# Kernel tuning notes

Hardware: AMD Instinct MI355X
Metric: run time of the kernel (lower is better)

Reference implementation:

```python
import jax, jax.numpy as jnp
import numpy as np

N = 100000   # nodes
E = 625000   # edges
D = 128      # feature / embedding dim
C = 40       # num classes
BN_EPS = 1e-5
L2_EPS = 1e-12


def setup_inputs() -> dict:
    key = jax.random.key(0)
    ks = jax.random.split(key, 8)
    s = 1.0 / np.sqrt(D)
    return {
        "x": jax.random.normal(ks[0], (N, D), dtype=jnp.float32),
        "edge_index": jax.random.randint(ks[1], (2, E), 0, N, dtype=jnp.int64),
        "W1": jax.random.normal(ks[2], (D, D), dtype=jnp.float32) * s,
        "b1": jnp.zeros((D,), jnp.float32),
        "W2": jax.random.normal(ks[3], (D, D), dtype=jnp.float32) * s,
        "b2": jnp.zeros((D,), jnp.float32),
        "W3": jax.random.normal(ks[4], (D, D), dtype=jnp.float32) * s,
        "b3": jnp.zeros((D,), jnp.float32),
        "g1": jnp.ones((D,), jnp.float32), "be1": jnp.zeros((D,), jnp.float32),
        "g2": jnp.ones((D,), jnp.float32), "be2": jnp.zeros((D,), jnp.float32),
        "g3": jnp.ones((D,), jnp.float32), "be3": jnp.zeros((D,), jnp.float32),
        "Wout": jax.random.normal(ks[5], (D, C), dtype=jnp.float32) * s,
        "bout": jnp.zeros((C,), jnp.float32),
    }


def _gcn_norm(edge_index, n):
    # PyG GCNConv default: add self loops, symmetric normalization
    loop = jnp.arange(n)
    src = jnp.concatenate([edge_index[0], loop])
    dst = jnp.concatenate([edge_index[1], loop])
    deg = jax.ops.segment_sum(jnp.ones_like(src, dtype=jnp.float32), dst, num_segments=n)
    dinv = jnp.where(deg > 0, jax.lax.rsqrt(deg), 0.0)
    norm = dinv[src] * dinv[dst]  # [E+N]
    return src, dst, norm


def _gcn_conv(x, W, b, src, dst, norm, n):
    h = x @ W                                # [N, D]
    msg = h[src] * norm[:, None]             # gather, [E+N, D]
    out = jax.ops.segment_sum(msg, dst, num_segments=n)  # scatter-add
    return out + b


def _bn(x, g, b):
    mu = jnp.mean(x, axis=0)
    var = jnp.var(x, axis=0)
    return (x - mu) * jax.lax.rsqrt(var + BN_EPS) * g + b


def _l2norm(x):
    n = jnp.sqrt(jnp.sum(x * x, axis=1, keepdims=True))
    return x / jnp.maximum(n, L2_EPS)


def reference(x, edge_index, W1, b1, W2, b2, W3, b3,
              g1, be1, g2, be2, g3, be3, Wout, bout):
    n = x.shape[0]
    src, dst, norm = _gcn_norm(edge_index, n)

    h = jax.nn.relu(_bn(_gcn_conv(x, W1, b1, src, dst, norm, n), g1, be1))
    h = _l2norm(h)
    r = h
    h = jax.nn.relu(_bn(_gcn_conv(h, W2, b2, src, dst, norm, n), g2, be2))
    h = _l2norm(h + r)
    r = h
    h = jax.nn.relu(_bn(_gcn_conv(h, W3, b3, src, dst, norm, n), g3, be3))
    h = _l2norm(h + r)

    return h @ Wout + bout  # node classification logits [N, C]
```

## Files before the change

### kernel.cpp

```cpp
#include <hip/hip_runtime.h>
#include <math.h>

#define DD 128
#define COUT 40
#define BN_EPS 1e-5f
#define L2_EPS 1e-12f

typedef __attribute__((ext_vector_type(8))) short bf16x8;
typedef __attribute__((ext_vector_type(4))) float f32x4;

static __device__ inline unsigned short f2bf(float f) {
    unsigned int x = __float_as_uint(f);
    unsigned int r = (x + 0x7FFFu + ((x >> 16) & 1u)) >> 16;
    return (unsigned short)r;
}
static __device__ inline float bf2f(unsigned short u) {
    return __uint_as_float(((unsigned int)u) << 16);
}


__global__ void k_prep(const float* __restrict__ W1, const float* __restrict__ W2,
                       const float* __restrict__ W3, const float* __restrict__ Wout,
                       unsigned short* __restrict__ wb,
                       unsigned short* __restrict__ wob,
                       float* __restrict__ stats,
                       int* __restrict__ zbase, int zn) {
    int b = blockIdx.x;
    if (b < 24) {
        int wi = b >> 3;
        const float* W = (wi == 0) ? W1 : (wi == 1) ? W2 : W3;
        unsigned short* out = wb + wi * 16384;
        int idx = (b & 7) * 256 + threadIdx.x;
        int kc = idx >> 9;
        int cc = (idx >> 6) & 7;
        int lane = idx & 63;
        int n = cc * 16 + (lane & 15);
        int kb = kc * 32 + (lane >> 4) * 8;
        unsigned short tmp[8];
#pragma unroll
        for (int j = 0; j < 8; j++) tmp[j] = f2bf(W[(size_t)(kb + j) * DD + n]);
        *(uint4*)&out[(size_t)idx * 8] = *(const uint4*)tmp;
    } else if (b < 27) {
        int idx = (b - 24) * 256 + threadIdx.x;
        int kc = idx / 192;
        int rem = idx % 192;
        int cc = rem >> 6;
        int lane = rem & 63;
        int n = cc * 16 + (lane & 15);
        int kb = kc * 32 + (lane >> 4) * 8;
        unsigned short tmp[8];
#pragma unroll
        for (int j = 0; j < 8; j++)
            tmp[j] = (n < COUT) ? f2bf(Wout[(size_t)(kb + j) * COUT + n]) : 0;
        *(uint4*)&wob[(size_t)idx * 8] = *(const uint4*)tmp;
    } else if (b == 27) {
        stats[threadIdx.x] = 0.f;
        stats[256 + threadIdx.x] = 0.f;
        stats[512 + threadIdx.x] = 0.f;
    } else {
        int idx = (b - 28) * 2048 + threadIdx.x * 8;
        if (idx + 8 <= zn) {
            *(int4*)&zbase[idx] = make_int4(0, 0, 0, 0);
            *(int4*)&zbase[idx + 4] = make_int4(0, 0, 0, 0);
        }
    }
}

__global__ void k_hist(const int* ei, int E, int* deg) {
    int i = blockIdx.x * blockDim.x + threadIdx.x;
    if (i < E) atomicAdd(&deg[ei[E + i]], 1);
}

__global__ void k_scan_a(const int* deg, int* row_ptr, int* bsum, float* dinv, int n) {
    __shared__ int s[256];
    int t = threadIdx.x;
    int idx = blockIdx.x * 256 + t;
    int v = (idx < n) ? deg[idx] + 1 : 0;
    if (idx < n) dinv[idx] = rsqrtf((float)v);
    s[t] = v; __syncthreads();
    for (int off = 1; off < 256; off <<= 1) {
        int x = (t >= off) ? s[t - off] : 0;
        __syncthreads(); s[t] += x; __syncthreads();
    }
    if (idx <= n) row_ptr[idx] = s[t] - v;
    if (t == 255) bsum[blockIdx.x] = s[255];
}

__global__ void k_scan_b(const int* bsum, int* boff, int nb) {
    __shared__ int s[512];
    int t = threadIdx.x;
    int v = (t < nb) ? bsum[t] : 0;
    s[t] = v; __syncthreads();
    for (int off = 1; off < 512; off <<= 1) {
        int x = (t >= off) ? s[t - off] : 0;
        __syncthreads(); s[t] += x; __syncthreads();
    }
    if (t < nb) boff[t] = s[t] - v;
}

__global__ void k_fill(const int* ei, int E, int n, const int* row_ptr, const int* boff,
                       int* fill, int* colidx) {
    int i = blockIdx.x * blockDim.x + threadIdx.x;
    int total = E + n;
    if (i >= total) return;
    int u, v;
    if (i < E) { u = ei[i]; v = ei[E + i]; }
    else { u = i - E; v = u; }
    int p = atomicAdd(&fill[v], 1);
    int pos = row_ptr[v] + boff[v >> 8] + p;
    colidx[pos] = u;
}


__global__ __launch_bounds__(256) void k_gemm0(const float* __restrict__ A,
                                               const unsigned short* __restrict__ Wb,
                                               const float* __restrict__ dinv,
                                               unsigned short* __restrict__ C, int nrows) {
    __shared__ __align__(16) unsigned short Ws[16384];
    const int tid = threadIdx.x;
    for (int i = tid; i < 2048; i += 256)
        ((uint4*)Ws)[i] = ((const uint4*)Wb)[i];
    __syncthreads();

    const int wv = tid >> 6;
    const int lane = tid & 63;
    const int R0 = blockIdx.x * 64 + wv * 16;
    if (R0 >= nrows) return;
    const int m = lane & 15, q = lane >> 4;
    int rr = R0 + m; if (rr >= nrows) rr = nrows - 1;
    const float* Ar = A + (size_t)rr * DD + q * 8;

    bf16x8 af[4];
#pragma unroll
    for (int kc = 0; kc < 4; kc++) {
        float4 lo = *(const float4*)(Ar + kc * 32);
        float4 hi = *(const float4*)(Ar + kc * 32 + 4);
        unsigned short t[8];
        t[0] = f2bf(lo.x); t[1] = f2bf(lo.y); t[2] = f2bf(lo.z); t[3] = f2bf(lo.w);
        t[4] = f2bf(hi.x); t[5] = f2bf(hi.y); t[6] = f2bf(hi.z); t[7] = f2bf(hi.w);
        af[kc] = *(const bf16x8*)t;
    }

    f32x4 acc[8];
#pragma unroll
    for (int cc = 0; cc < 8; cc++) acc[cc] = (f32x4){0.f, 0.f, 0.f, 0.f};
#pragma unroll
    for (int kc = 0; kc < 4; kc++)
#pragma unroll
        for (int cc = 0; cc < 8; cc++) {
            bf16x8 b = *(const bf16x8*)&Ws[(size_t)((kc * 8 + cc) * 64 + lane) * 8];
            acc[cc] = __builtin_amdgcn_mfma_f32_16x16x32_bf16(af[kc], b, acc[cc], 0, 0, 0);
        }

    float dr[4];
#pragma unroll
    for (int i = 0; i < 4; i++) {
        int r = R0 + q * 4 + i;
        dr[i] = (r < nrows) ? dinv[r] : 0.f;
    }
#pragma unroll
    for (int cc = 0; cc < 8; cc++)
#pragma unroll
        for (int i = 0; i < 4; i++) {
            int r = R0 + q * 4 + i;
            if (r < nrows) C[(size_t)r * DD + cc * 16 + m] = f2bf(acc[cc][i] * dr[i]);
        }
}

__global__ void k_agg(const unsigned short* __restrict__ lin, const int* __restrict__ row_ptr,
                      const int* __restrict__ boff, const int* __restrict__ colidx,
                      const float* __restrict__ dinv, const float* __restrict__ bias,
                      unsigned short* __restrict__ outb, int n) {
    int lane = threadIdx.x;
    int half = lane >> 5;
    int li = lane & 31;
    int v = blockIdx.x * 8 + threadIdx.y * 2 + half;
    if (v >= n) return;
    int c = li * 4;
    int s = row_ptr[v] + boff[v >> 8];
    int e = row_ptr[v + 1] + boff[(v + 1) >> 8];
    float dv = dinv[v];
    float4 a0 = make_float4(0.f, 0.f, 0.f, 0.f);
    float4 a1 = make_float4(0.f, 0.f, 0.f, 0.f);
    float4 a2 = make_float4(0.f, 0.f, 0.f, 0.f);
    float4 a3 = make_float4(0.f, 0.f, 0.f, 0.f);
    int j = s;
    for (; j + 3 < e; j += 4) {
        int u0 = colidx[j], u1 = colidx[j + 1], u2 = colidx[j + 2], u3 = colidx[j + 3];
        ushort4 t0 = *(const ushort4*)&lin[(size_t)u0 * DD + c];
        ushort4 t1 = *(const ushort4*)&lin[(size_t)u1 * DD + c];
        ushort4 t2 = *(const ushort4*)&lin[(size_t)u2 * DD + c];
        ushort4 t3 = *(const ushort4*)&lin[(size_t)u3 * DD + c];
        a0.x += bf2f(t0.x); a0.y += bf2f(t0.y); a0.z += bf2f(t0.z); a0.w += bf2f(t0.w);
        a1.x += bf2f(t1.x); a1.y += bf2f(t1.y); a1.z += bf2f(t1.z); a1.w += bf2f(t1.w);
        a2.x += bf2f(t2.x); a2.y += bf2f(t2.y); a2.z += bf2f(t2.z); a2.w += bf2f(t2.w);
        a3.x += bf2f(t3.x); a3.y += bf2f(t3.y); a3.z += bf2f(t3.z); a3.w += bf2f(t3.w);
    }
    for (; j < e; ++j) {
        int u = colidx[j];
        ushort4 t = *(const ushort4*)&lin[(size_t)u * DD + c];
        a0.x += bf2f(t.x); a0.y += bf2f(t.y); a0.z += bf2f(t.z); a0.w += bf2f(t.w);
    }
    float4 bi = *(const float4*)&bias[c];
    float ox = bi.x + dv * (a0.x + a1.x + a2.x + a3.x);
    float oy = bi.y + dv * (a0.y + a1.y + a2.y + a3.y);
    float oz = bi.z + dv * (a0.z + a1.z + a2.z + a3.z);
    float ow = bi.w + dv * (a0.w + a1.w + a2.w + a3.w);
    ushort4 o;
    o.x = f2bf(ox); o.y = f2bf(oy); o.z = f2bf(oz); o.w = f2bf(ow);
    *(ushort4*)&outb[(size_t)v * DD + c] = o;
}

__global__ __launch_bounds__(256) void k_bnstats(const unsigned short* __restrict__ X, int n,
                                                 float* __restrict__ stats) {
    int cg = (threadIdx.x & 31) * 4;
    int rg = threadIdx.x >> 5;
    float s0 = 0, s1 = 0, s2 = 0, s3 = 0;
    float q0 = 0, q1 = 0, q2 = 0, q3 = 0;
    for (int r = blockIdx.x * 8 + rg; r < n; r += gridDim.x * 8) {
        ushort4 xv = *(const ushort4*)&X[(size_t)r * DD + cg];
        float x0 = bf2f(xv.x), x1 = bf2f(xv.y), x2 = bf2f(xv.z), x3 = bf2f(xv.w);
        s0 += x0; s1 += x1; s2 += x2; s3 += x3;
        q0 += x0 * x0; q1 += x1 * x1; q2 += x2 * x2; q3 += x3 * x3;
    }
    __shared__ float sh[8][128];
    __shared__ float qh[8][128];
    sh[rg][cg] = s0; sh[rg][cg + 1] = s1; sh[rg][cg + 2] = s2; sh[rg][cg + 3] = s3;
    qh[rg][cg] = q0; qh[rg][cg + 1] = q1; qh[rg][cg + 2] = q2; qh[rg][cg + 3] = q3;
    __syncthreads();
    if (threadIdx.x < 128) {
        float a = 0, b = 0;
        for (int g = 0; g < 8; g++) { a += sh[g][threadIdx.x]; b += qh[g][threadIdx.x]; }
        atomicAdd(&stats[threadIdx.x], a);
        atomicAdd(&stats[128 + threadIdx.x], b);
    }
}

template <bool HAS_RES>
__global__ __launch_bounds__(256) void k_fused(const unsigned short* __restrict__ aggX,
                                               const float* __restrict__ stats,
                                               const float* __restrict__ g,
                                               const float* __restrict__ be, float inv_n,
                                               const unsigned short* __restrict__ resb,
                                               const unsigned short* __restrict__ Wb,
                                               const float* __restrict__ dinv,
                                               unsigned short* __restrict__ hbf_out,
                                               unsigned short* __restrict__ linb_out,
                                               int nrows) {
    __shared__ __align__(16) unsigned short Ws[16384];
    __shared__ float ssl[256];
    const int tid = threadIdx.x;
    for (int i = tid; i < 2048; i += 256)
        ((uint4*)Ws)[i] = ((const uint4*)Wb)[i];
    if (tid < 128) {
        float mu = stats[tid] * inv_n;
        float var = stats[128 + tid] * inv_n - mu * mu;
        float sc = g[tid] * rsqrtf(var + BN_EPS);
        ssl[tid] = sc;
        ssl[128 + tid] = be[tid] - mu * sc;
    }
    __syncthreads();

    const int wv = tid >> 6;
    const int lane = tid & 63;
    const int R0 = blockIdx.x * 64 + wv * 16;
    if (R0 >= nrows) return;
    const int m = lane & 15, q = lane >> 4;
    int rr = R0 + m; if (rr >= nrows) rr = nrows - 1;
    const unsigned short* Ar = aggX + (size_t)rr * DD + q * 8;
    const unsigned short* Rr = HAS_RES ? resb + (size_t)rr * DD + q * 8 : nullptr;

    float y[4][8];
    float sq = 0.f;
#pragma unroll
    for (int kc = 0; kc < 4; kc++) {
        ushort4 lo = *(const ushort4*)(Ar + kc * 32);
        ushort4 hi = *(const ushort4*)(Ar + kc * 32 + 4);
        unsigned short av[8] = {lo.x, lo.y, lo.z, lo.w, hi.x, hi.y, hi.z, hi.w};
        int c0 = kc * 32 + q * 8;
        float4 sc0 = *(const float4*)&ssl[c0];
        float4 sc1 = *(const float4*)&ssl[c0 + 4];
        float4 sh0 = *(const float4*)&ssl[128 + c0];
        float4 sh1 = *(const float4*)&ssl[128 + c0 + 4];
        float scv[8] = {sc0.x, sc0.y, sc0.z, sc0.w, sc1.x, sc1.y, sc1.z, sc1.w};
        float shv[8] = {sh0.x, sh0.y, sh0.z, sh0.w, sh1.x, sh1.y, sh1.z, sh1.w};
        if (HAS_RES) {
            ushort4 rl = *(const ushort4*)(Rr + kc * 32);
            ushort4 rh = *(const ushort4*)(Rr + kc * 32 + 4);
            unsigned short rv[8] = {rl.x, rl.y, rl.z, rl.w, rh.x, rh.y, rh.z, rh.w};
#pragma unroll
            for (int j = 0; j < 8; j++) {
                float yy = fmaxf(bf2f(av[j]) * scv[j] + shv[j], 0.f) + bf2f(rv[j]);
                y[kc][j] = yy; sq += yy * yy;
            }
        } else {
#pragma unroll
            for (int j = 0; j < 8; j++) {
                float yy = fmaxf(bf2f(av[j]) * scv[j] + shv[j], 0.f);
                y[kc][j] = yy; sq += yy * yy;
            }
        }
    }
    sq += __shfl_xor(sq, 16, 64);
    sq += __shfl_xor(sq, 32, 64);
    float inv = 1.f / fmaxf(sqrtf(sq), L2_EPS);

    bf16x8 af[4];
#pragma unroll
    for (int kc = 0; kc < 4; kc++) {
        unsigned short t[8];
#pragma unroll
        for (int j = 0; j < 8; j++) t[j] = f2bf(y[kc][j] * inv);
        af[kc] = *(const bf16x8*)t;
        *(bf16x8*)&hbf_out[(size_t)rr * DD + q * 8 + kc * 32] = af[kc];
    }

    f32x4 acc[8];
#pragma unroll
    for (int cc = 0; cc < 8; cc++) acc[cc] = (f32x4){0.f, 0.f, 0.f, 0.f};
#pragma unroll
    for (int kc = 0; kc < 4; kc++)
#pragma unroll
        for (int cc = 0; cc < 8; cc++) {
            bf16x8 b = *(const bf16x8*)&Ws[(size_t)((kc * 8 + cc) * 64 + lane) * 8];
            acc[cc] = __builtin_amdgcn_mfma_f32_16x16x32_bf16(af[kc], b, acc[cc], 0, 0, 0);
        }

    float dr[4];
#pragma unroll
    for (int i = 0; i < 4; i++) {
        int r = R0 + q * 4 + i;
        dr[i] = (r < nrows) ? dinv[r] : 0.f;
    }
#pragma unroll
    for (int cc = 0; cc < 8; cc++)
#pragma unroll
        for (int i = 0; i < 4; i++) {
            int r = R0 + q * 4 + i;
            if (r < nrows) linb_out[(size_t)r * DD + cc * 16 + m] = f2bf(acc[cc][i] * dr[i]);
        }
}

__global__ __launch_bounds__(256) void k_outfused(const unsigned short* __restrict__ aggX,
                                                  const float* __restrict__ stats,
                                                  const float* __restrict__ g,
                                                  const float* __restrict__ be, float inv_n,
                                                  const unsigned short* __restrict__ resb,
                                                  const unsigned short* __restrict__ wob,
                                                  const float* __restrict__ bout,
                                                  float* __restrict__ C, int nrows) {
    __shared__ __align__(16) unsigned short Ws[6144];
    __shared__ float ssl[256];
    const int tid = threadIdx.x;
    for (int i = tid; i < 768; i += 256)
        ((uint4*)Ws)[i] = ((const uint4*)wob)[i];
    if (tid < 128) {
        float mu = stats[tid] * inv_n;
        float var = stats[128 + tid] * inv_n - mu * mu;
        float sc = g[tid] * rsqrtf(var + BN_EPS);
        ssl[tid] = sc;
        ssl[128 + tid] = be[tid] - mu * sc;
    }
    __syncthreads();

    const int wv = tid >> 6;
    const int lane = tid & 63;
    const int R0 = blockIdx.x * 64 + wv * 16;
    if (R0 >= nrows) return;
    const int m = lane & 15, q = lane >> 4;
    int rr = R0 + m; if (rr >= nrows) rr = nrows - 1;
    const unsigned short* Ar = aggX + (size_t)rr * DD + q * 8;
    const unsigned short* Rr = resb + (size_t)rr * DD + q * 8;

    float y[4][8];
    float sq = 0.f;
#pragma unroll
    for (int kc = 0; kc < 4; kc++) {
        ushort4 lo = *(const ushort4*)(Ar + kc * 32);
        ushort4 hi = *(const ushort4*)(Ar + kc * 32 + 4);
        ushort4 rl = *(const ushort4*)(Rr + kc * 32);
        ushort4 rh = *(const ushort4*)(Rr + kc * 32 + 4);
        unsigned short av[8] = {lo.x, lo.y, lo.z, lo.w, hi.x, hi.y, hi.z, hi.w};
        unsigned short rv[8] = {rl.x, rl.y, rl.z, rl.w, rh.x, rh.y, rh.z, rh.w};
        int c0 = kc * 32 + q * 8;
        float4 sc0 = *(const float4*)&ssl[c0];
        float4 sc1 = *(const float4*)&ssl[c0 + 4];
        float4 sh0 = *(const float4*)&ssl[128 + c0];
        float4 sh1 = *(const float4*)&ssl[128 + c0 + 4];
        float scv[8] = {sc0.x, sc0.y, sc0.z, sc0.w, sc1.x, sc1.y, sc1.z, sc1.w};
        float shv[8] = {sh0.x, sh0.y, sh0.z, sh0.w, sh1.x, sh1.y, sh1.z, sh1.w};
#pragma unroll
        for (int j = 0; j < 8; j++) {
            float yy = fmaxf(bf2f(av[j]) * scv[j] + shv[j], 0.f) + bf2f(rv[j]);
            y[kc][j] = yy; sq += yy * yy;
        }
    }
    sq += __shfl_xor(sq, 16, 64);
    sq += __shfl_xor(sq, 32, 64);
    float inv = 1.f / fmaxf(sqrtf(sq), L2_EPS);

    bf16x8 af[4];
#pragma unroll
    for (int kc = 0; kc < 4; kc++) {
        unsigned short t[8];
#pragma unroll
        for (int j = 0; j < 8; j++) t[j] = f2bf(y[kc][j] * inv);
        af[kc] = *(const bf16x8*)t;
    }

    f32x4 acc[3];
#pragma unroll
    for (int cc = 0; cc < 3; cc++) acc[cc] = (f32x4){0.f, 0.f, 0.f, 0.f};
#pragma unroll
    for (int kc = 0; kc < 4; kc++)
#pragma unroll
        for (int cc = 0; cc < 3; cc++) {
            bf16x8 b = *(const bf16x8*)&Ws[(size_t)((kc * 3 + cc) * 64 + lane) * 8];
            acc[cc] = __builtin_amdgcn_mfma_f32_16x16x32_bf16(af[kc], b, acc[cc], 0, 0, 0);
        }

#pragma unroll
    for (int cc = 0; cc < 3; cc++) {
        int col = cc * 16 + m;
        if (col < COUT) {
            float bb = bout[col];
#pragma unroll
            for (int i = 0; i < 4; i++) {
                int r = R0 + q * 4 + i;
                if (r < nrows) C[(size_t)r * COUT + col] = acc[cc][i] + bb;
            }
        }
    }
}


extern "C" void kernel_launch(void* const* d_in, const int* in_sizes, int n_in,
                              void* d_out, int out_size, void* d_ws, size_t ws_size,
                              hipStream_t stream) {
    const float* x    = (const float*)d_in[0];
    const int*   ei   = (const int*)d_in[1];
    const float* W1   = (const float*)d_in[2];
    const float* b1   = (const float*)d_in[3];
    const float* W2   = (const float*)d_in[4];
    const float* b2   = (const float*)d_in[5];
    const float* W3   = (const float*)d_in[6];
    const float* b3   = (const float*)d_in[7];
    const float* g1   = (const float*)d_in[8];
    const float* be1  = (const float*)d_in[9];
    const float* g2   = (const float*)d_in[10];
    const float* be2  = (const float*)d_in[11];
    const float* g3   = (const float*)d_in[12];
    const float* be3  = (const float*)d_in[13];
    const float* Wout = (const float*)d_in[14];
    const float* bout = (const float*)d_in[15];
    float* out = (float*)d_out;

    const int N = in_sizes[0] / DD;
    const int E = in_sizes[1] / 2;
    const int NNZ = E + N;

    char* w = (char*)d_ws;
    unsigned short* linb = (unsigned short*)w; w += (size_t)N * DD * sizeof(unsigned short);
    unsigned short* aggA = (unsigned short*)w; w += (size_t)N * DD * sizeof(unsigned short);
    unsigned short* aggB = (unsigned short*)w; w += (size_t)N * DD * sizeof(unsigned short);
    unsigned short* hbf1 = (unsigned short*)w; w += (size_t)N * DD * sizeof(unsigned short);
    unsigned short* hbf2 = (unsigned short*)w; w += (size_t)N * DD * sizeof(unsigned short);
    unsigned short* wb   = (unsigned short*)w; w += 3 * 16384 * sizeof(unsigned short);
    unsigned short* wob  = (unsigned short*)w; w += 6144 * sizeof(unsigned short);
    int* colidx  = (int*)w;                    w += (size_t)NNZ * sizeof(int);
    int* deg     = (int*)w;                    w += (size_t)N * sizeof(int);
    int* fill    = (int*)w;                    w += (size_t)N * sizeof(int);
    int* row_ptr = (int*)w;                    w += (size_t)(N + 1) * sizeof(int);
    float* dinv  = (float*)w;                  w += (size_t)N * sizeof(float);
    int* bsum    = (int*)w;                    w += 512 * sizeof(int);
    int* boff    = (int*)w;                    w += 512 * sizeof(int);
    float* stats = (float*)w;                  w += 768 * sizeof(float);

    const int NB = (N + 1 + 255) / 256;
    const int STATS_GRID = 128;
    const int ZN = 2 * N;
    const int ZBLK = (ZN + 2047) / 2048;

    k_prep<<<28 + ZBLK, 256, 0, stream>>>(W1, W2, W3, Wout, wb, wob, stats, deg, ZN);
    k_hist<<<(E + 255) / 256, 256, 0, stream>>>(ei, E, deg);
    k_scan_a<<<NB, 256, 0, stream>>>(deg, row_ptr, bsum, dinv, N);
    k_scan_b<<<1, 512, 0, stream>>>(bsum, boff, NB);
    k_fill<<<(NNZ + 255) / 256, 256, 0, stream>>>(ei, E, N, row_ptr, boff, fill, colidx);

    int gemmGrid = (N + 63) / 64;
    dim3 aggGrid((N + 7) / 8);
    dim3 aggBlk(64, 4);
    float inv_n = 1.0f / (float)N;

    k_gemm0<<<gemmGrid, 256, 0, stream>>>(x, wb, dinv, linb, N);
    k_agg<<<aggGrid, aggBlk, 0, stream>>>(linb, row_ptr, boff, colidx, dinv, b1, aggA, N);
    k_bnstats<<<STATS_GRID, 256, 0, stream>>>(aggA, N, stats);
    k_fused<false><<<gemmGrid, 256, 0, stream>>>(aggA, stats, g1, be1, inv_n,
                                                 nullptr, wb + 16384, dinv, hbf1, linb, N);
    k_agg<<<aggGrid, aggBlk, 0, stream>>>(linb, row_ptr, boff, colidx, dinv, b2, aggB, N);
    k_bnstats<<<STATS_GRID, 256, 0, stream>>>(aggB, N, stats + 256);
    k_fused<true><<<gemmGrid, 256, 0, stream>>>(aggB, stats + 256, g2, be2, inv_n,
                                                hbf1, wb + 32768, dinv, hbf2, linb, N);
    k_agg<<<aggGrid, aggBlk, 0, stream>>>(linb, row_ptr, boff, colidx, dinv, b3, aggA, N);
    k_bnstats<<<STATS_GRID, 256, 0, stream>>>(aggA, N, stats + 512);
    k_outfused<<<gemmGrid, 256, 0, stream>>>(aggA, stats + 512, g3, be3, inv_n,
                                             hbf2, wob, bout, out, N);
}
```

Before: 483.0 us.

## Merge all GCN stages into one cooperative persistent kernel with grid syncs

Replaces the sequence of roughly fifteen separate launches (prep, histogram, scans, fill, GEMM, aggregation, BN stats, fused layers) with a single cooperative kernel. It runs grid-stride stages separated by grid-wide barriers. BN statistics are now accumulated inside the aggregation stage through shared-memory atomics, which removes the separate stats passes over the aggregated features. This cuts launch overhead and one full read of the features per layer. In exchange it adds grid-sync costs, limits the grid to occupancy times the CU count, and makes host-side device property queries on every call.

```diff
diff --git a/kernel.cpp b/kernel.cpp
--- a/kernel.cpp
+++ b/kernel.cpp
@@ -1,5 +1,8 @@
 #include <hip/hip_runtime.h>
+#include <hip/hip_cooperative_groups.h>
 #include <math.h>
+
+namespace cg = cooperative_groups;
 
 #define DD 128
 #define COUT 40
@@ -18,240 +21,96 @@
     return __uint_as_float(((unsigned int)u) << 16);
 }
 
-
-__global__ void k_prep(const float* __restrict__ W1, const float* __restrict__ W2,
-                       const float* __restrict__ W3, const float* __restrict__ Wout,
-                       unsigned short* __restrict__ wb,
-                       unsigned short* __restrict__ wob,
-                       float* __restrict__ stats,
-                       int* __restrict__ zbase, int zn) {
-    int b = blockIdx.x;
-    if (b < 24) {
-        int wi = b >> 3;
-        const float* W = (wi == 0) ? W1 : (wi == 1) ? W2 : W3;
-        unsigned short* out = wb + wi * 16384;
-        int idx = (b & 7) * 256 + threadIdx.x;
-        int kc = idx >> 9;
-        int cc = (idx >> 6) & 7;
-        int lane = idx & 63;
-        int n = cc * 16 + (lane & 15);
-        int kb = kc * 32 + (lane >> 4) * 8;
-        unsigned short tmp[8];
-#pragma unroll
-        for (int j = 0; j < 8; j++) tmp[j] = f2bf(W[(size_t)(kb + j) * DD + n]);
-        *(uint4*)&out[(size_t)idx * 8] = *(const uint4*)tmp;
-    } else if (b < 27) {
-        int idx = (b - 24) * 256 + threadIdx.x;
-        int kc = idx / 192;
-        int rem = idx % 192;
-        int cc = rem >> 6;
-        int lane = rem & 63;
-        int n = cc * 16 + (lane & 15);
-        int kb = kc * 32 + (lane >> 4) * 8;
-        unsigned short tmp[8];
-#pragma unroll
-        for (int j = 0; j < 8; j++)
-            tmp[j] = (n < COUT) ? f2bf(Wout[(size_t)(kb + j) * COUT + n]) : 0;
-        *(uint4*)&wob[(size_t)idx * 8] = *(const uint4*)tmp;
-    } else if (b == 27) {
-        stats[threadIdx.x] = 0.f;
-        stats[256 + threadIdx.x] = 0.f;
-        stats[512 + threadIdx.x] = 0.f;
-    } else {
-        int idx = (b - 28) * 2048 + threadIdx.x * 8;
-        if (idx + 8 <= zn) {
-            *(int4*)&zbase[idx] = make_int4(0, 0, 0, 0);
-            *(int4*)&zbase[idx + 4] = make_int4(0, 0, 0, 0);
-        }
-    }
-}
-
-__global__ void k_hist(const int* ei, int E, int* deg) {
-    int i = blockIdx.x * blockDim.x + threadIdx.x;
-    if (i < E) atomicAdd(&deg[ei[E + i]], 1);
-}
-
-__global__ void k_scan_a(const int* deg, int* row_ptr, int* bsum, float* dinv, int n) {
-    __shared__ int s[256];
-    int t = threadIdx.x;
-    int idx = blockIdx.x * 256 + t;
-    int v = (idx < n) ? deg[idx] + 1 : 0;
-    if (idx < n) dinv[idx] = rsqrtf((float)v);
-    s[t] = v; __syncthreads();
-    for (int off = 1; off < 256; off <<= 1) {
-        int x = (t >= off) ? s[t - off] : 0;
-        __syncthreads(); s[t] += x; __syncthreads();
-    }
-    if (idx <= n) row_ptr[idx] = s[t] - v;
-    if (t == 255) bsum[blockIdx.x] = s[255];
-}
-
-__global__ void k_scan_b(const int* bsum, int* boff, int nb) {
-    __shared__ int s[512];
-    int t = threadIdx.x;
-    int v = (t < nb) ? bsum[t] : 0;
-    s[t] = v; __syncthreads();
-    for (int off = 1; off < 512; off <<= 1) {
-        int x = (t >= off) ? s[t - off] : 0;
-        __syncthreads(); s[t] += x; __syncthreads();
-    }
-    if (t < nb) boff[t] = s[t] - v;
-}
-
-__global__ void k_fill(const int* ei, int E, int n, const int* row_ptr, const int* boff,
-                       int* fill, int* colidx) {
-    int i = blockIdx.x * blockDim.x + threadIdx.x;
-    int total = E + n;
-    if (i >= total) return;
-    int u, v;
-    if (i < E) { u = ei[i]; v = ei[E + i]; }
-    else { u = i - E; v = u; }
-    int p = atomicAdd(&fill[v], 1);
-    int pos = row_ptr[v] + boff[v >> 8] + p;
-    colidx[pos] = u;
-}
-
-
-__global__ __launch_bounds__(256) void k_gemm0(const float* __restrict__ A,
-                                               const unsigned short* __restrict__ Wb,
-                                               const float* __restrict__ dinv,
-                                               unsigned short* __restrict__ C, int nrows) {
-    __shared__ __align__(16) unsigned short Ws[16384];
+struct MegaParams {
+    const float* x; const int* ei;
+    const float *W1, *b1, *W2, *b2, *W3, *b3;
+    const float *g1, *be1, *g2, *be2, *g3, *be3;
+    const float *Wout, *bout;
+    float* out;
+    unsigned short *linb, *aggA, *aggB, *hbf1, *hbf2, *wb, *wob;
+    int *colidx, *deg, *fill, *row_ptr;
+    float* dinv;
+    int *bsum, *boff;
+    float* stats;
+    int N, E, NB;
+};
+
+
+static __device__ __forceinline__ void st_agg(const unsigned short* __restrict__ lin,
+                                              const int* __restrict__ row_ptr,
+                                              const int* __restrict__ boff,
+                                              const int* __restrict__ colidx,
+                                              const float* __restrict__ dinv,
+                                              const float* __restrict__ bias,
+                                              unsigned short* __restrict__ outb,
+                                              float* __restrict__ gstats,
+                                              float* lstats, int N) {
     const int tid = threadIdx.x;
-    for (int i = tid; i < 2048; i += 256)
-        ((uint4*)Ws)[i] = ((const uint4*)Wb)[i];
+    lstats[tid] = 0.f;
     __syncthreads();
-
-    const int wv = tid >> 6;
-    const int lane = tid & 63;
-    const int R0 = blockIdx.x * 64 + wv * 16;
-    if (R0 >= nrows) return;
-    const int m = lane & 15, q = lane >> 4;
-    int rr = R0 + m; if (rr >= nrows) rr = nrows - 1;
-    const float* Ar = A + (size_t)rr * DD + q * 8;
-
-    bf16x8 af[4];
-#pragma unroll
-    for (int kc = 0; kc < 4; kc++) {
-        float4 lo = *(const float4*)(Ar + kc * 32);
-        float4 hi = *(const float4*)(Ar + kc * 32 + 4);
-        unsigned short t[8];
-        t[0] = f2bf(lo.x); t[1] = f2bf(lo.y); t[2] = f2bf(lo.z); t[3] = f2bf(lo.w);
-        t[4] = f2bf(hi.x); t[5] = f2bf(hi.y); t[6] = f2bf(hi.z); t[7] = f2bf(hi.w);
-        af[kc] = *(const bf16x8*)t;
-    }
-
-    f32x4 acc[8];
-#pragma unroll
-    for (int cc = 0; cc < 8; cc++) acc[cc] = (f32x4){0.f, 0.f, 0.f, 0.f};
-#pragma unroll
-    for (int kc = 0; kc < 4; kc++)
-#pragma unroll
-        for (int cc = 0; cc < 8; cc++) {
-            bf16x8 b = *(const bf16x8*)&Ws[(size_t)((kc * 8 + cc) * 64 + lane) * 8];
-            acc[cc] = __builtin_amdgcn_mfma_f32_16x16x32_bf16(af[kc], b, acc[cc], 0, 0, 0);
-        }
-
-    float dr[4];
-#pragma unroll
-    for (int i = 0; i < 4; i++) {
-        int r = R0 + q * 4 + i;
-        dr[i] = (r < nrows) ? dinv[r] : 0.f;
-    }
-#pragma unroll
-    for (int cc = 0; cc < 8; cc++)
-#pragma unroll
-        for (int i = 0; i < 4; i++) {
-            int r = R0 + q * 4 + i;
-            if (r < nrows) C[(size_t)r * DD + cc * 16 + m] = f2bf(acc[cc][i] * dr[i]);
-        }
-}
-
-__global__ void k_agg(const unsigned short* __restrict__ lin, const int* __restrict__ row_ptr,
-                      const int* __restrict__ boff, const int* __restrict__ colidx,
-                      const float* __restrict__ dinv, const float* __restrict__ bias,
-                      unsigned short* __restrict__ outb, int n) {
-    int lane = threadIdx.x;
-    int half = lane >> 5;
-    int li = lane & 31;
-    int v = blockIdx.x * 8 + threadIdx.y * 2 + half;
-    if (v >= n) return;
-    int c = li * 4;
-    int s = row_ptr[v] + boff[v >> 8];
-    int e = row_ptr[v + 1] + boff[(v + 1) >> 8];
-    float dv = dinv[v];
-    float4 a0 = make_float4(0.f, 0.f, 0.f, 0.f);
-    float4 a1 = make_float4(0.f, 0.f, 0.f, 0.f);
-    float4 a2 = make_float4(0.f, 0.f, 0.f, 0.f);
-    float4 a3 = make_float4(0.f, 0.f, 0.f, 0.f);
-    int j = s;
-    for (; j + 3 < e; j += 4) {
-        int u0 = colidx[j], u1 = colidx[j + 1], u2 = colidx[j + 2], u3 = colidx[j + 3];
-        ushort4 t0 = *(const ushort4*)&lin[(size_t)u0 * DD + c];
-        ushort4 t1 = *(const ushort4*)&lin[(size_t)u1 * DD + c];
-        ushort4 t2 = *(const ushort4*)&lin[(size_t)u2 * DD + c];
-        ushort4 t3 = *(const ushort4*)&lin[(size_t)u3 * DD + c];
-        a0.x += bf2f(t0.x); a0.y += bf2f(t0.y); a0.z += bf2f(t0.z); a0.w += bf2f(t0.w);
-        a1.x += bf2f(t1.x); a1.y += bf2f(t1.y); a1.z += bf2f(t1.z); a1.w += bf2f(t1.w);
-        a2.x += bf2f(t2.x); a2.y += bf2f(t2.y); a2.z += bf2f(t2.z); a2.w += bf2f(t2.w);
-        a3.x += bf2f(t3.x); a3.y += bf2f(t3.y); a3.z += bf2f(t3.z); a3.w += bf2f(t3.w);
-    }
-    for (; j < e; ++j) {
-        int u = colidx[j];
-        ushort4 t = *(const ushort4*)&lin[(size_t)u * DD + c];
-        a0.x += bf2f(t.x); a0.y += bf2f(t.y); a0.z += bf2f(t.z); a0.w += bf2f(t.w);
-    }
-    float4 bi = *(const float4*)&bias[c];
-    float ox = bi.x + dv * (a0.x + a1.x + a2.x + a3.x);
-    float oy = bi.y + dv * (a0.y + a1.y + a2.y + a3.y);
-    float oz = bi.z + dv * (a0.z + a1.z + a2.z + a3.z);
-    float ow = bi.w + dv * (a0.w + a1.w + a2.w + a3.w);
-    ushort4 o;
-    o.x = f2bf(ox); o.y = f2bf(oy); o.z = f2bf(oz); o.w = f2bf(ow);
-    *(ushort4*)&outb[(size_t)v * DD + c] = o;
-}
-
-__global__ __launch_bounds__(256) void k_bnstats(const unsigned short* __restrict__ X, int n,
-                                                 float* __restrict__ stats) {
-    int cg = (threadIdx.x & 31) * 4;
-    int rg = threadIdx.x >> 5;
-    float s0 = 0, s1 = 0, s2 = 0, s3 = 0;
-    float q0 = 0, q1 = 0, q2 = 0, q3 = 0;
-    for (int r = blockIdx.x * 8 + rg; r < n; r += gridDim.x * 8) {
-        ushort4 xv = *(const ushort4*)&X[(size_t)r * DD + cg];
-        float x0 = bf2f(xv.x), x1 = bf2f(xv.y), x2 = bf2f(xv.z), x3 = bf2f(xv.w);
-        s0 += x0; s1 += x1; s2 += x2; s3 += x3;
-        q0 += x0 * x0; q1 += x1 * x1; q2 += x2 * x2; q3 += x3 * x3;
-    }
-    __shared__ float sh[8][128];
-    __shared__ float qh[8][128];
-    sh[rg][cg] = s0; sh[rg][cg + 1] = s1; sh[rg][cg + 2] = s2; sh[rg][cg + 3] = s3;
-    qh[rg][cg] = q0; qh[rg][cg + 1] = q1; qh[rg][cg + 2] = q2; qh[rg][cg + 3] = q3;
+    const int slot = (tid >> 6) * 2 + ((tid & 63) >> 5);
+    const int c = (tid & 31) * 4;
+    float s0 = 0, s1 = 0, s2 = 0, s3 = 0, q0 = 0, q1 = 0, q2 = 0, q3 = 0;
+    const int VB = (N + 7) / 8;
+    for (int vb = blockIdx.x; vb < VB; vb += gridDim.x) {
+        int v = vb * 8 + slot;
+        if (v >= N) continue;
+        int s = row_ptr[v] + boff[v >> 8];
+        int e = row_ptr[v + 1] + boff[(v + 1) >> 8];
+        float dv = dinv[v];
+        float4 a0 = make_float4(0.f, 0.f, 0.f, 0.f);
+        float4 a1 = make_float4(0.f, 0.f, 0.f, 0.f);
+        float4 a2 = make_float4(0.f, 0.f, 0.f, 0.f);
+        float4 a3 = make_float4(0.f, 0.f, 0.f, 0.f);
+        int j = s;
+        for (; j + 3 < e; j += 4) {
+            int u0 = colidx[j], u1 = colidx[j + 1], u2 = colidx[j + 2], u3 = colidx[j + 3];
+            ushort4 t0 = *(const ushort4*)&lin[(size_t)u0 * DD + c];
+            ushort4 t1 = *(const ushort4*)&lin[(size_t)u1 * DD + c];
+            ushort4 t2 = *(const ushort4*)&lin[(size_t)u2 * DD + c];
+            ushort4 t3 = *(const ushort4*)&lin[(size_t)u3 * DD + c];
+            a0.x += bf2f(t0.x); a0.y += bf2f(t0.y); a0.z += bf2f(t0.z); a0.w += bf2f(t0.w);
+            a1.x += bf2f(t1.x); a1.y += bf2f(t1.y); a1.z += bf2f(t1.z); a1.w += bf2f(t1.w);
+            a2.x += bf2f(t2.x); a2.y += bf2f(t2.y); a2.z += bf2f(t2.z); a2.w += bf2f(t2.w);
+            a3.x += bf2f(t3.x); a3.y += bf2f(t3.y); a3.z += bf2f(t3.z); a3.w += bf2f(t3.w);
+        }
+        for (; j < e; ++j) {
+            int u = colidx[j];
+            ushort4 t = *(const ushort4*)&lin[(size_t)u * DD + c];
+            a0.x += bf2f(t.x); a0.y += bf2f(t.y); a0.z += bf2f(t.z); a0.w += bf2f(t.w);
+        }
+        float4 bi = *(const float4*)&bias[c];
+        float ox = bi.x + dv * (a0.x + a1.x + a2.x + a3.x);
+        float oy = bi.y + dv * (a0.y + a1.y + a2.y + a3.y);
+        float oz = bi.z + dv * (a0.z + a1.z + a2.z + a3.z);
+        float ow = bi.w + dv * (a0.w + a1.w + a2.w + a3.w);
+        s0 += ox; s1 += oy; s2 += oz; s3 += ow;
+        q0 += ox * ox; q1 += oy * oy; q2 += oz * oz; q3 += ow * ow;
+        ushort4 o;
+        o.x = f2bf(ox); o.y = f2bf(oy); o.z = f2bf(oz); o.w = f2bf(ow);
+        *(ushort4*)&outb[(size_t)v * DD + c] = o;
+    }
+    atomicAdd(&lstats[c], s0); atomicAdd(&lstats[c + 1], s1);
+    atomicAdd(&lstats[c + 2], s2); atomicAdd(&lstats[c + 3], s3);
+    atomicAdd(&lstats[128 + c], q0); atomicAdd(&lstats[128 + c + 1], q1);
+    atomicAdd(&lstats[128 + c + 2], q2); atomicAdd(&lstats[128 + c + 3], q3);
     __syncthreads();
-    if (threadIdx.x < 128) {
-        float a = 0, b = 0;
-        for (int g = 0; g < 8; g++) { a += sh[g][threadIdx.x]; b += qh[g][threadIdx.x]; }
-        atomicAdd(&stats[threadIdx.x], a);
-        atomicAdd(&stats[128 + threadIdx.x], b);
-    }
+    atomicAdd(&gstats[tid], lstats[tid]);
 }
 
 template <bool HAS_RES>
-__global__ __launch_bounds__(256) void k_fused(const unsigned short* __restrict__ aggX,
-                                               const float* __restrict__ stats,
-                                               const float* __restrict__ g,
-                                               const float* __restrict__ be, float inv_n,
-                                               const unsigned short* __restrict__ resb,
-                                               const unsigned short* __restrict__ Wb,
-                                               const float* __restrict__ dinv,
-                                               unsigned short* __restrict__ hbf_out,
-                                               unsigned short* __restrict__ linb_out,
-                                               int nrows) {
-    __shared__ __align__(16) unsigned short Ws[16384];
-    __shared__ float ssl[256];
+static __device__ __forceinline__ void st_fused(const unsigned short* __restrict__ aggX,
+                                                const float* __restrict__ stats,
+                                                const float* __restrict__ g,
+                                                const float* __restrict__ be, float inv_n,
+                                                const unsigned short* __restrict__ resb,
+                                                const unsigned short* __restrict__ Wb,
+                                                const float* __restrict__ dinv,
+                                                unsigned short* __restrict__ hbf_out,
+                                                unsigned short* __restrict__ linb_out,
+                                                unsigned short* Ws, float* ssl, int N) {
     const int tid = threadIdx.x;
-    for (int i = tid; i < 2048; i += 256)
-        ((uint4*)Ws)[i] = ((const uint4*)Wb)[i];
+    for (int i = tid; i < 2048; i += 256) ((uint4*)Ws)[i] = ((const uint4*)Wb)[i];
     if (tid < 128) {
         float mu = stats[tid] * inv_n;
         float var = stats[128 + tid] * inv_n - mu * mu;
@@ -260,174 +119,304 @@
         ssl[128 + tid] = be[tid] - mu * sc;
     }
     __syncthreads();
-
-    const int wv = tid >> 6;
-    const int lane = tid & 63;
-    const int R0 = blockIdx.x * 64 + wv * 16;
-    if (R0 >= nrows) return;
-    const int m = lane & 15, q = lane >> 4;
-    int rr = R0 + m; if (rr >= nrows) rr = nrows - 1;
-    const unsigned short* Ar = aggX + (size_t)rr * DD + q * 8;
-    const unsigned short* Rr = HAS_RES ? resb + (size_t)rr * DD + q * 8 : nullptr;
-
-    float y[4][8];
-    float sq = 0.f;
-#pragma unroll
-    for (int kc = 0; kc < 4; kc++) {
-        ushort4 lo = *(const ushort4*)(Ar + kc * 32);
-        ushort4 hi = *(const ushort4*)(Ar + kc * 32 + 4);
-        unsigned short av[8] = {lo.x, lo.y, lo.z, lo.w, hi.x, hi.y, hi.z, hi.w};
-        int c0 = kc * 32 + q * 8;
-        float4 sc0 = *(const float4*)&ssl[c0];
-        float4 sc1 = *(const float4*)&ssl[c0 + 4];
-        float4 sh0 = *(const float4*)&ssl[128 + c0];
-        float4 sh1 = *(const float4*)&ssl[128 + c0 + 4];
-        float scv[8] = {sc0.x, sc0.y, sc0.z, sc0.w, sc1.x, sc1.y, sc1.z, sc1.w};
-        float shv[8] = {sh0.x, sh0.y, sh0.z, sh0.w, sh1.x, sh1.y, sh1.z, sh1.w};
-        if (HAS_RES) {
-            ushort4 rl = *(const ushort4*)(Rr + kc * 32);
-            ushort4 rh = *(const ushort4*)(Rr + kc * 32 + 4);
-            unsigned short rv[8] = {rl.x, rl.y, rl.z, rl.w, rh.x, rh.y, rh.z, rh.w};
-#pragma unroll
-            for (int j = 0; j < 8; j++) {
-                float yy = fmaxf(bf2f(av[j]) * scv[j] + shv[j], 0.f) + bf2f(rv[j]);
-                y[kc][j] = yy; sq += yy * yy;
-            }
-        } else {
-#pragma unroll
-            for (int j = 0; j < 8; j++) {
-                float yy = fmaxf(bf2f(av[j]) * scv[j] + shv[j], 0.f);
-                y[kc][j] = yy; sq += yy * yy;
-            }
-        }
-    }
-    sq += __shfl_xor(sq, 16, 64);
-    sq += __shfl_xor(sq, 32, 64);
-    float inv = 1.f / fmaxf(sqrtf(sq), L2_EPS);
-
-    bf16x8 af[4];
-#pragma unroll
-    for (int kc = 0; kc < 4; kc++) {
-        unsigned short t[8];
-#pragma unroll
-        for (int j = 0; j < 8; j++) t[j] = f2bf(y[kc][j] * inv);
-        af[kc] = *(const bf16x8*)t;
-        *(bf16x8*)&hbf_out[(size_t)rr * DD + q * 8 + kc * 32] = af[kc];
-    }
-
-    f32x4 acc[8];
-#pragma unroll
-    for (int cc = 0; cc < 8; cc++) acc[cc] = (f32x4){0.f, 0.f, 0.f, 0.f};
-#pragma unroll
-    for (int kc = 0; kc < 4; kc++)
-#pragma unroll
-        for (int cc = 0; cc < 8; cc++) {
-            bf16x8 b = *(const bf16x8*)&Ws[(size_t)((kc * 8 + cc) * 64 + lane) * 8];
-            acc[cc] = __builtin_amdgcn_mfma_f32_16x16x32_bf16(af[kc], b, acc[cc], 0, 0, 0);
-        }
-
-    float dr[4];
-#pragma unroll
-    for (int i = 0; i < 4; i++) {
-        int r = R0 + q * 4 + i;
-        dr[i] = (r < nrows) ? dinv[r] : 0.f;
-    }
-#pragma unroll
-    for (int cc = 0; cc < 8; cc++)
+    const int wv = tid >> 6, lane = tid & 63, m = lane & 15, q = lane >> 4;
+    const int NC = (N + 63) / 64;
+    for (int cb = blockIdx.x; cb < NC; cb += gridDim.x) {
+        int R0 = cb * 64 + wv * 16;
+        if (R0 >= N) continue;
+        int rr = R0 + m; if (rr >= N) rr = N - 1;
+        const unsigned short* Ar = aggX + (size_t)rr * DD + q * 8;
+        const unsigned short* Rr = HAS_RES ? resb + (size_t)rr * DD + q * 8 : nullptr;
+        float y[4][8];
+        float sq = 0.f;
+#pragma unroll
+        for (int kc = 0; kc < 4; kc++) {
+            ushort4 lo = *(const ushort4*)(Ar + kc * 32);
+            ushort4 hi = *(const ushort4*)(Ar + kc * 32 + 4);
+            unsigned short av[8] = {lo.x, lo.y, lo.z, lo.w, hi.x, hi.y, hi.z, hi.w};
+            int c0 = kc * 32 + q * 8;
+            float4 sc0 = *(const float4*)&ssl[c0];
+            float4 sc1 = *(const float4*)&ssl[c0 + 4];
+            float4 sh0 = *(const float4*)&ssl[128 + c0];
+            float4 sh1 = *(const float4*)&ssl[128 + c0 + 4];
+            float scv[8] = {sc0.x, sc0.y, sc0.z, sc0.w, sc1.x, sc1.y, sc1.z, sc1.w};
+            float shv[8] = {sh0.x, sh0.y, sh0.z, sh0.w, sh1.x, sh1.y, sh1.z, sh1.w};
+            if (HAS_RES) {
+                ushort4 rl = *(const ushort4*)(Rr + kc * 32);
+                ushort4 rh = *(const ushort4*)(Rr + kc * 32 + 4);
+                unsigned short rv[8] = {rl.x, rl.y, rl.z, rl.w, rh.x, rh.y, rh.z, rh.w};
+#pragma unroll
+                for (int j = 0; j < 8; j++) {
+                    float yy = fmaxf(bf2f(av[j]) * scv[j] + shv[j], 0.f) + bf2f(rv[j]);
+                    y[kc][j] = yy; sq += yy * yy;
+                }
+            } else {
+#pragma unroll
+                for (int j = 0; j < 8; j++) {
+                    float yy = fmaxf(bf2f(av[j]) * scv[j] + shv[j], 0.f);
+                    y[kc][j] = yy; sq += yy * yy;
+                }
+            }
+        }
+        sq += __shfl_xor(sq, 16, 64);
+        sq += __shfl_xor(sq, 32, 64);
+        float inv = 1.f / fmaxf(sqrtf(sq), L2_EPS);
+        bf16x8 af[4];
+#pragma unroll
+        for (int kc = 0; kc < 4; kc++) {
+            unsigned short t[8];
+#pragma unroll
+            for (int j = 0; j < 8; j++) t[j] = f2bf(y[kc][j] * inv);
+            af[kc] = *(const bf16x8*)t;
+            *(bf16x8*)&hbf_out[(size_t)rr * DD + q * 8 + kc * 32] = af[kc];
+        }
+        f32x4 acc[8];
+#pragma unroll
+        for (int cc = 0; cc < 8; cc++) acc[cc] = (f32x4){0.f, 0.f, 0.f, 0.f};
+#pragma unroll
+        for (int kc = 0; kc < 4; kc++)
+#pragma unroll
+            for (int cc = 0; cc < 8; cc++) {
+                bf16x8 b = *(const bf16x8*)&Ws[(size_t)((kc * 8 + cc) * 64 + lane) * 8];
+                acc[cc] = __builtin_amdgcn_mfma_f32_16x16x32_bf16(af[kc], b, acc[cc], 0, 0, 0);
+            }
+        float dr[4];
 #pragma unroll
         for (int i = 0; i < 4; i++) {
             int r = R0 + q * 4 + i;
-            if (r < nrows) linb_out[(size_t)r * DD + cc * 16 + m] = f2bf(acc[cc][i] * dr[i]);
-        }
-}
-
-__global__ __launch_bounds__(256) void k_outfused(const unsigned short* __restrict__ aggX,
-                                                  const float* __restrict__ stats,
-                                                  const float* __restrict__ g,
-                                                  const float* __restrict__ be, float inv_n,
-                                                  const unsigned short* __restrict__ resb,
-                                                  const unsigned short* __restrict__ wob,
-                                                  const float* __restrict__ bout,
-                                                  float* __restrict__ C, int nrows) {
-    __shared__ __align__(16) unsigned short Ws[6144];
-    __shared__ float ssl[256];
-    const int tid = threadIdx.x;
-    for (int i = tid; i < 768; i += 256)
-        ((uint4*)Ws)[i] = ((const uint4*)wob)[i];
-    if (tid < 128) {
-        float mu = stats[tid] * inv_n;
-        float var = stats[128 + tid] * inv_n - mu * mu;
-        float sc = g[tid] * rsqrtf(var + BN_EPS);
-        ssl[tid] = sc;
-        ssl[128 + tid] = be[tid] - mu * sc;
-    }
-    __syncthreads();
-
-    const int wv = tid >> 6;
-    const int lane = tid & 63;
-    const int R0 = blockIdx.x * 64 + wv * 16;
-    if (R0 >= nrows) return;
-    const int m = lane & 15, q = lane >> 4;
-    int rr = R0 + m; if (rr >= nrows) rr = nrows - 1;
-    const unsigned short* Ar = aggX + (size_t)rr * DD + q * 8;
-    const unsigned short* Rr = resb + (size_t)rr * DD + q * 8;
-
-    float y[4][8];
-    float sq = 0.f;
-#pragma unroll
-    for (int kc = 0; kc < 4; kc++) {
-        ushort4 lo = *(const ushort4*)(Ar + kc * 32);
-        ushort4 hi = *(const ushort4*)(Ar + kc * 32 + 4);
-        ushort4 rl = *(const ushort4*)(Rr + kc * 32);
-        ushort4 rh = *(const ushort4*)(Rr + kc * 32 + 4);
-        unsigned short av[8] = {lo.x, lo.y, lo.z, lo.w, hi.x, hi.y, hi.z, hi.w};
-        unsigned short rv[8] = {rl.x, rl.y, rl.z, rl.w, rh.x, rh.y, rh.z, rh.w};
-        int c0 = kc * 32 + q * 8;
-        float4 sc0 = *(const float4*)&ssl[c0];
-        float4 sc1 = *(const float4*)&ssl[c0 + 4];
-        float4 sh0 = *(const float4*)&ssl[128 + c0];
-        float4 sh1 = *(const float4*)&ssl[128 + c0 + 4];
-        float scv[8] = {sc0.x, sc0.y, sc0.z, sc0.w, sc1.x, sc1.y, sc1.z, sc1.w};
-        float shv[8] = {sh0.x, sh0.y, sh0.z, sh0.w, sh1.x, sh1.y, sh1.z, sh1.w};
-#pragma unroll
-        for (int j = 0; j < 8; j++) {
-            float yy = fmaxf(bf2f(av[j]) * scv[j] + shv[j], 0.f) + bf2f(rv[j]);
-            y[kc][j] = yy; sq += yy * yy;
-        }
-    }
-    sq += __shfl_xor(sq, 16, 64);
-    sq += __shfl_xor(sq, 32, 64);
-    float inv = 1.f / fmaxf(sqrtf(sq), L2_EPS);
-
-    bf16x8 af[4];
-#pragma unroll
-    for (int kc = 0; kc < 4; kc++) {
-        unsigned short t[8];
-#pragma unroll
-        for (int j = 0; j < 8; j++) t[j] = f2bf(y[kc][j] * inv);
-        af[kc] = *(const bf16x8*)t;
-    }
-
-    f32x4 acc[3];
-#pragma unroll
-    for (int cc = 0; cc < 3; cc++) acc[cc] = (f32x4){0.f, 0.f, 0.f, 0.f};
-#pragma unroll
-    for (int kc = 0; kc < 4; kc++)
-#pragma unroll
-        for (int cc = 0; cc < 3; cc++) {
-            bf16x8 b = *(const bf16x8*)&Ws[(size_t)((kc * 3 + cc) * 64 + lane) * 8];
-            acc[cc] = __builtin_amdgcn_mfma_f32_16x16x32_bf16(af[kc], b, acc[cc], 0, 0, 0);
-        }
-
-#pragma unroll
-    for (int cc = 0; cc < 3; cc++) {
-        int col = cc * 16 + m;
-        if (col < COUT) {
-            float bb = bout[col];
+            dr[i] = (r < N) ? dinv[r] : 0.f;
+        }
+#pragma unroll
+        for (int cc = 0; cc < 8; cc++)
 #pragma unroll
             for (int i = 0; i < 4; i++) {
                 int r = R0 + q * 4 + i;
-                if (r < nrows) C[(size_t)r * COUT + col] = acc[cc][i] + bb;
+                if (r < N) linb_out[(size_t)r * DD + cc * 16 + m] = f2bf(acc[cc][i] * dr[i]);
+            }
+    }
+}
+
+
+__global__ __launch_bounds__(256) void k_mega(MegaParams p) {
+    cg::grid_group grid = cg::this_grid();
+    const int tid = threadIdx.x;
+    const int gid = blockIdx.x * 256 + tid;
+    const int gsz = gridDim.x * 256;
+
+    __shared__ __align__(16) unsigned short Ws[16384];
+    __shared__ __align__(16) float ssl[256];
+    int* si = (int*)ssl;
+
+    for (int i = gid; i < 6144; i += gsz) {
+        int wi = i >> 11;
+        int idx = i & 2047;
+        const float* W = (wi == 0) ? p.W1 : (wi == 1) ? p.W2 : p.W3;
+        int kc = idx >> 9, cc = (idx >> 6) & 7, lane = idx & 63;
+        int n = cc * 16 + (lane & 15);
+        int kb = kc * 32 + (lane >> 4) * 8;
+        unsigned short tmp[8];
+#pragma unroll
+        for (int j = 0; j < 8; j++) tmp[j] = f2bf(W[(size_t)(kb + j) * DD + n]);
+        *(uint4*)&p.wb[(size_t)(wi * 16384 + idx * 8)] = *(const uint4*)tmp;
+    }
+    for (int i = gid; i < 768; i += gsz) {
+        int kc = i / 192, rem = i % 192;
+        int cc = rem >> 6, lane = rem & 63;
+        int n = cc * 16 + (lane & 15);
+        int kb = kc * 32 + (lane >> 4) * 8;
+        unsigned short tmp[8];
+#pragma unroll
+        for (int j = 0; j < 8; j++)
+            tmp[j] = (n < COUT) ? f2bf(p.Wout[(size_t)(kb + j) * COUT + n]) : 0;
+        *(uint4*)&p.wob[(size_t)i * 8] = *(const uint4*)tmp;
+    }
+    for (int i = gid; i < 768; i += gsz) p.stats[i] = 0.f;
+    int zn4 = (2 * p.N) / 4;
+    for (int i = gid; i < zn4; i += gsz) ((int4*)p.deg)[i] = make_int4(0, 0, 0, 0);
+    grid.sync();
+
+    for (int i = gid; i < p.E; i += gsz) atomicAdd(&p.deg[p.ei[p.E + i]], 1);
+    grid.sync();
+
+    for (int b = blockIdx.x; b < p.NB; b += gridDim.x) {
+        int idx = b * 256 + tid;
+        int v = (idx < p.N) ? p.deg[idx] + 1 : 0;
+        if (idx < p.N) p.dinv[idx] = rsqrtf((float)v);
+        si[tid] = v; __syncthreads();
+        for (int off = 1; off < 256; off <<= 1) {
+            int xx = (tid >= off) ? si[tid - off] : 0;
+            __syncthreads(); si[tid] += xx; __syncthreads();
+        }
+        if (idx <= p.N) p.row_ptr[idx] = si[tid] - v;
+        if (tid == 255) p.bsum[b] = si[255];
+        __syncthreads();
+    }
+    grid.sync();
+
+    if (blockIdx.x == 0) {
+        int carry = 0;
+        for (int t0 = 0; t0 < p.NB; t0 += 256) {
+            int i = t0 + tid;
+            int v = (i < p.NB) ? p.bsum[i] : 0;
+            si[tid] = v; __syncthreads();
+            for (int off = 1; off < 256; off <<= 1) {
+                int xx = (tid >= off) ? si[tid - off] : 0;
+                __syncthreads(); si[tid] += xx; __syncthreads();
+            }
+            if (i < p.NB) p.boff[i] = si[tid] - v + carry;
+            carry += si[255];
+            __syncthreads();
+        }
+    }
+    grid.sync();
+
+    {
+        int total = p.E + p.N;
+        for (int i = gid; i < total; i += gsz) {
+            int u, v;
+            if (i < p.E) { u = p.ei[i]; v = p.ei[p.E + i]; }
+            else { u = i - p.E; v = u; }
+            int pp = atomicAdd(&p.fill[v], 1);
+            p.colidx[p.row_ptr[v] + p.boff[v >> 8] + pp] = u;
+        }
+    }
+    grid.sync();
+
+    {
+        for (int i = tid; i < 2048; i += 256) ((uint4*)Ws)[i] = ((const uint4*)p.wb)[i];
+        __syncthreads();
+        const int wv = tid >> 6, lane = tid & 63, m = lane & 15, q = lane >> 4;
+        const int NC = (p.N + 63) / 64;
+        for (int cb = blockIdx.x; cb < NC; cb += gridDim.x) {
+            int R0 = cb * 64 + wv * 16;
+            if (R0 >= p.N) continue;
+            int rr = R0 + m; if (rr >= p.N) rr = p.N - 1;
+            const float* Ar = p.x + (size_t)rr * DD + q * 8;
+            bf16x8 af[4];
+#pragma unroll
+            for (int kc = 0; kc < 4; kc++) {
+                float4 lo = *(const float4*)(Ar + kc * 32);
+                float4 hi = *(const float4*)(Ar + kc * 32 + 4);
+                unsigned short t[8];
+                t[0] = f2bf(lo.x); t[1] = f2bf(lo.y); t[2] = f2bf(lo.z); t[3] = f2bf(lo.w);
+                t[4] = f2bf(hi.x); t[5] = f2bf(hi.y); t[6] = f2bf(hi.z); t[7] = f2bf(hi.w);
+                af[kc] = *(const bf16x8*)t;
+            }
+            f32x4 acc[8];
+#pragma unroll
+            for (int cc = 0; cc < 8; cc++) acc[cc] = (f32x4){0.f, 0.f, 0.f, 0.f};
+#pragma unroll
+            for (int kc = 0; kc < 4; kc++)
+#pragma unroll
+                for (int cc = 0; cc < 8; cc++) {
+                    bf16x8 b = *(const bf16x8*)&Ws[(size_t)((kc * 8 + cc) * 64 + lane) * 8];
+                    acc[cc] = __builtin_amdgcn_mfma_f32_16x16x32_bf16(af[kc], b, acc[cc], 0, 0, 0);
+                }
+            float dr[4];
+#pragma unroll
+            for (int i = 0; i < 4; i++) {
+                int r = R0 + q * 4 + i;
+                dr[i] = (r < p.N) ? p.dinv[r] : 0.f;
+            }
+#pragma unroll
+            for (int cc = 0; cc < 8; cc++)
+#pragma unroll
+                for (int i = 0; i < 4; i++) {
+                    int r = R0 + q * 4 + i;
+                    if (r < p.N) p.linb[(size_t)r * DD + cc * 16 + m] = f2bf(acc[cc][i] * dr[i]);
+                }
+        }
+    }
+    grid.sync();
+
+    float inv_n = 1.0f / (float)p.N;
+
+    st_agg(p.linb, p.row_ptr, p.boff, p.colidx, p.dinv, p.b1, p.aggA, p.stats, ssl, p.N);
+    grid.sync();
+    st_fused<false>(p.aggA, p.stats, p.g1, p.be1, inv_n, nullptr,
+                    p.wb + 16384, p.dinv, p.hbf1, p.linb, Ws, ssl, p.N);
+    grid.sync();
+    st_agg(p.linb, p.row_ptr, p.boff, p.colidx, p.dinv, p.b2, p.aggB, p.stats + 256, ssl, p.N);
+    grid.sync();
+    st_fused<true>(p.aggB, p.stats + 256, p.g2, p.be2, inv_n, p.hbf1,
+                   p.wb + 32768, p.dinv, p.hbf2, p.linb, Ws, ssl, p.N);
+    grid.sync();
+    st_agg(p.linb, p.row_ptr, p.boff, p.colidx, p.dinv, p.b3, p.aggA, p.stats + 512, ssl, p.N);
+    grid.sync();
+
+    {
+        for (int i = tid; i < 768; i += 256) ((uint4*)Ws)[i] = ((const uint4*)p.wob)[i];
+        if (tid < 128) {
+            float mu = p.stats[512 + tid] * inv_n;
+            float var = p.stats[512 + 128 + tid] * inv_n - mu * mu;
+            float sc = p.g3[tid] * rsqrtf(var + BN_EPS);
+            ssl[tid] = sc;
+            ssl[128 + tid] = p.be3[tid] - mu * sc;
+        }
+        __syncthreads();
+        const int wv = tid >> 6, lane = tid & 63, m = lane & 15, q = lane >> 4;
+        const int NC = (p.N + 63) / 64;
+        for (int cb = blockIdx.x; cb < NC; cb += gridDim.x) {
+            int R0 = cb * 64 + wv * 16;
+            if (R0 >= p.N) continue;
+            int rr = R0 + m; if (rr >= p.N) rr = p.N - 1;
+            const unsigned short* Ar = p.aggA + (size_t)rr * DD + q * 8;
+            const unsigned short* Rr = p.hbf2 + (size_t)rr * DD + q * 8;
+            float y[4][8];
+            float sq = 0.f;
+#pragma unroll
+            for (int kc = 0; kc < 4; kc++) {
+                ushort4 lo = *(const ushort4*)(Ar + kc * 32);
+                ushort4 hi = *(const ushort4*)(Ar + kc * 32 + 4);
+                ushort4 rl = *(const ushort4*)(Rr + kc * 32);
+                ushort4 rh = *(const ushort4*)(Rr + kc * 32 + 4);
+                unsigned short av[8] = {lo.x, lo.y, lo.z, lo.w, hi.x, hi.y, hi.z, hi.w};
+                unsigned short rv[8] = {rl.x, rl.y, rl.z, rl.w, rh.x, rh.y, rh.z, rh.w};
+                int c0 = kc * 32 + q * 8;
+                float4 sc0 = *(const float4*)&ssl[c0];
+                float4 sc1 = *(const float4*)&ssl[c0 + 4];
+                float4 sh0 = *(const float4*)&ssl[128 + c0];
+                float4 sh1 = *(const float4*)&ssl[128 + c0 + 4];
+                float scv[8] = {sc0.x, sc0.y, sc0.z, sc0.w, sc1.x, sc1.y, sc1.z, sc1.w};
+                float shv[8] = {sh0.x, sh0.y, sh0.z, sh0.w, sh1.x, sh1.y, sh1.z, sh1.w};
+#pragma unroll
+                for (int j = 0; j < 8; j++) {
+                    float yy = fmaxf(bf2f(av[j]) * scv[j] + shv[j], 0.f) + bf2f(rv[j]);
+                    y[kc][j] = yy; sq += yy * yy;
+                }
+            }
+            sq += __shfl_xor(sq, 16, 64);
+            sq += __shfl_xor(sq, 32, 64);
+            float inv = 1.f / fmaxf(sqrtf(sq), L2_EPS);
+            bf16x8 af[4];
+#pragma unroll
+            for (int kc = 0; kc < 4; kc++) {
+                unsigned short t[8];
+#pragma unroll
+                for (int j = 0; j < 8; j++) t[j] = f2bf(y[kc][j] * inv);
+                af[kc] = *(const bf16x8*)t;
+            }
+            f32x4 acc[3];
+#pragma unroll
+            for (int cc = 0; cc < 3; cc++) acc[cc] = (f32x4){0.f, 0.f, 0.f, 0.f};
+#pragma unroll
+            for (int kc = 0; kc < 4; kc++)
+#pragma unroll
+                for (int cc = 0; cc < 3; cc++) {
+                    bf16x8 b = *(const bf16x8*)&Ws[(size_t)((kc * 3 + cc) * 64 + lane) * 8];
+                    acc[cc] = __builtin_amdgcn_mfma_f32_16x16x32_bf16(af[kc], b, acc[cc], 0, 0, 0);
+                }
+#pragma unroll
+            for (int cc = 0; cc < 3; cc++) {
+                int col = cc * 16 + m;
+                if (col < COUT) {
+                    float bb = p.bout[col];
+#pragma unroll
+                    for (int i = 0; i < 4; i++) {
+                        int r = R0 + q * 4 + i;
+                        if (r < p.N) p.out[(size_t)r * COUT + col] = acc[cc][i] + bb;
+                    }
+                }
             }
         }
     }
@@ -437,72 +426,50 @@
 extern "C" void kernel_launch(void* const* d_in, const int* in_sizes, int n_in,
                               void* d_out, int out_size, void* d_ws, size_t ws_size,
                               hipStream_t stream) {
-    const float* x    = (const float*)d_in[0];
-    const int*   ei   = (const int*)d_in[1];
-    const float* W1   = (const float*)d_in[2];
-    const float* b1   = (const float*)d_in[3];
-    const float* W2   = (const float*)d_in[4];
-    const float* b2   = (const float*)d_in[5];
-    const float* W3   = (const float*)d_in[6];
-    const float* b3   = (const float*)d_in[7];
-    const float* g1   = (const float*)d_in[8];
-    const float* be1  = (const float*)d_in[9];
-    const float* g2   = (const float*)d_in[10];
-    const float* be2  = (const float*)d_in[11];
-    const float* g3   = (const float*)d_in[12];
-    const float* be3  = (const float*)d_in[13];
-    const float* Wout = (const float*)d_in[14];
-    const float* bout = (const float*)d_in[15];
-    float* out = (float*)d_out;
+    MegaParams p;
+    p.x    = (const float*)d_in[0];
+    p.ei   = (const int*)d_in[1];
+    p.W1   = (const float*)d_in[2];  p.b1  = (const float*)d_in[3];
+    p.W2   = (const float*)d_in[4];  p.b2  = (const float*)d_in[5];
+    p.W3   = (const float*)d_in[6];  p.b3  = (const float*)d_in[7];
+    p.g1   = (const float*)d_in[8];  p.be1 = (const float*)d_in[9];
+    p.g2   = (const float*)d_in[10]; p.be2 = (const float*)d_in[11];
+    p.g3   = (const float*)d_in[12]; p.be3 = (const float*)d_in[13];
+    p.Wout = (const float*)d_in[14]; p.bout = (const float*)d_in[15];
+    p.out  = (float*)d_out;
 
     const int N = in_sizes[0] / DD;
     const int E = in_sizes[1] / 2;
     const int NNZ = E + N;
+    p.N = N; p.E = E; p.NB = (N + 1 + 255) / 256;
 
     char* w = (char*)d_ws;
-    unsigned short* linb = (unsigned short*)w; w += (size_t)N * DD * sizeof(unsigned short);
-    unsigned short* aggA = (unsigned short*)w; w += (size_t)N * DD * sizeof(unsigned short);
-    unsigned short* aggB = (unsigned short*)w; w += (size_t)N * DD * sizeof(unsigned short);
-    unsigned short* hbf1 = (unsigned short*)w; w += (size_t)N * DD * sizeof(unsigned short);
-    unsigned short* hbf2 = (unsigned short*)w; w += (size_t)N * DD * sizeof(unsigned short);
-    unsigned short* wb   = (unsigned short*)w; w += 3 * 16384 * sizeof(unsigned short);
-    unsigned short* wob  = (unsigned short*)w; w += 6144 * sizeof(unsigned short);
-    int* colidx  = (int*)w;                    w += (size_t)NNZ * sizeof(int);
-    int* deg     = (int*)w;                    w += (size_t)N * sizeof(int);
-    int* fill    = (int*)w;                    w += (size_t)N * sizeof(int);
-    int* row_ptr = (int*)w;                    w += (size_t)(N + 1) * sizeof(int);
-    float* dinv  = (float*)w;                  w += (size_t)N * sizeof(float);
-    int* bsum    = (int*)w;                    w += 512 * sizeof(int);
-    int* boff    = (int*)w;                    w += 512 * sizeof(int);
-    float* stats = (float*)w;                  w += 768 * sizeof(float);
-
-    const int NB = (N + 1 + 255) / 256;
-    const int STATS_GRID = 128;
-    const int ZN = 2 * N;
-    const int ZBLK = (ZN + 2047) / 2048;
-
-    k_prep<<<28 + ZBLK, 256, 0, stream>>>(W1, W2, W3, Wout, wb, wob, stats, deg, ZN);
-    k_hist<<<(E + 255) / 256, 256, 0, stream>>>(ei, E, deg);
-    k_scan_a<<<NB, 256, 0, stream>>>(deg, row_ptr, bsum, dinv, N);
-    k_scan_b<<<1, 512, 0, stream>>>(bsum, boff, NB);
-    k_fill<<<(NNZ + 255) / 256, 256, 0, stream>>>(ei, E, N, row_ptr, boff, fill, colidx);
-
-    int gemmGrid = (N + 63) / 64;
-    dim3 aggGrid((N + 7) / 8);
-    dim3 aggBlk(64, 4);
-    float inv_n = 1.0f / (float)N;
-
-    k_gemm0<<<gemmGrid, 256, 0, stream>>>(x, wb, dinv, linb, N);
-    k_agg<<<aggGrid, aggBlk, 0, stream>>>(linb, row_ptr, boff, colidx, dinv, b1, aggA, N);
-    k_bnstats<<<STATS_GRID, 256, 0, stream>>>(aggA, N, stats);
-    k_fused<false><<<gemmGrid, 256, 0, stream>>>(aggA, stats, g1, be1, inv_n,
-                                                 nullptr, wb + 16384, dinv, hbf1, linb, N);
-    k_agg<<<aggGrid, aggBlk, 0, stream>>>(linb, row_ptr, boff, colidx, dinv, b2, aggB, N);
-    k_bnstats<<<STATS_GRID, 256, 0, stream>>>(aggB, N, stats + 256);
-    k_fused<true><<<gemmGrid, 256, 0, stream>>>(aggB, stats + 256, g2, be2, inv_n,
-                                                hbf1, wb + 32768, dinv, hbf2, linb, N);
-    k_agg<<<aggGrid, aggBlk, 0, stream>>>(linb, row_ptr, boff, colidx, dinv, b3, aggA, N);
-    k_bnstats<<<STATS_GRID, 256, 0, stream>>>(aggA, N, stats + 512);
-    k_outfused<<<gemmGrid, 256, 0, stream>>>(aggA, stats + 512, g3, be3, inv_n,
-                                             hbf2, wob, bout, out, N);
-}
+    p.linb = (unsigned short*)w;  w += (size_t)N * DD * sizeof(unsigned short);
+    p.aggA = (unsigned short*)w;  w += (size_t)N * DD * sizeof(unsigned short);
+    p.aggB = (unsigned short*)w;  w += (size_t)N * DD * sizeof(unsigned short);
+    p.hbf1 = (unsigned short*)w;  w += (size_t)N * DD * sizeof(unsigned short);
+    p.hbf2 = (unsigned short*)w;  w += (size_t)N * DD * sizeof(unsigned short);
+    p.wb   = (unsigned short*)w;  w += 3 * 16384 * sizeof(unsigned short);
+    p.wob  = (unsigned short*)w;  w += 6144 * sizeof(unsigned short);
+    p.colidx = (int*)w;           w += (size_t)NNZ * sizeof(int);
+    p.deg  = (int*)w;             w += (size_t)N * sizeof(int);
+    p.fill = (int*)w;             w += (size_t)N * sizeof(int);
+    p.row_ptr = (int*)w;          w += (size_t)(N + 1) * sizeof(int);
+    p.dinv = (float*)w;           w += (size_t)N * sizeof(float);
+    p.bsum = (int*)w;             w += 512 * sizeof(int);
+    p.boff = (int*)w;             w += 512 * sizeof(int);
+    p.stats = (float*)w;          w += 768 * sizeof(float);
+
+    int occ = 0;
+    hipOccupancyMaxActiveBlocksPerMultiprocessor(&occ, (const void*)k_mega, 256, 0);
+    if (occ < 1) occ = 1;
+    int dev = 0;
+    hipGetDevice(&dev);
+    hipDeviceProp_t props;
+    hipGetDeviceProperties(&props, dev);
+    int G = occ * props.multiProcessorCount;
+    if (G < 1) G = 256;
+
+    void* args[] = {&p};
+    hipLaunchCooperativeKernel((void*)k_mega, dim3(G), dim3(256), args, 0, stream);
+}
```

After: 1.131 ms. 2.34x slower.
